# Performance work log

Measured on AMD Instinct MI355X. Metric: run time of the kernel, lower is better.

The kernel has to match this reference:

```python
import jax, jax.numpy as jnp
import numpy as np

HEADS = 8
DIM_HEAD = 64
SCALE = DIM_HEAD ** -0.5  # q scaling
EPS = 1e-5  # channel LayerNorm eps (float32)


def setup_inputs() -> dict:
    key = jax.random.key(0)
    ks = jax.random.split(key, 4)
    B, C, H, W = 8, 256, 64, 64
    hd = HEADS * DIM_HEAD  # 512
    x = jax.random.normal(ks[0], (B, C, H, W), dtype=jnp.float32)
    w_qkv = jax.random.normal(ks[1], (3 * hd, C), dtype=jnp.float32) * 0.02  # 1x1 conv, no bias
    w_out = jax.random.normal(ks[2], (C, hd), dtype=jnp.float32) * 0.02     # 1x1 conv
    b_out = jax.random.normal(ks[3], (C,), dtype=jnp.float32) * 0.02
    g_ln = jnp.ones((C,), dtype=jnp.float32)  # LayerNorm gamma
    return {"x": x, "w_qkv": w_qkv, "w_out": w_out, "b_out": b_out, "g_ln": g_ln}


def reference(x, w_qkv, w_out, b_out, g_ln):
    B, C, H, W = x.shape
    n = H * W
    hd = HEADS * DIM_HEAD
    # 1x1 conv == per-pixel matmul: [B,C,H,W] x [3hd,C] -> [B,3hd,H,W]
    qkv = jnp.einsum('bchw,oc->bohw', x, w_qkv).reshape(B, 3, HEADS, DIM_HEAD, n)
    q, k, v = qkv[:, 0], qkv[:, 1], qkv[:, 2]  # each [B,h,d,n]
    q = jax.nn.softmax(q, axis=-2) * SCALE      # softmax over head-dim d
    k = jax.nn.softmax(k, axis=-1)              # softmax over spatial n
    v = v / n
    context = jnp.einsum('bhdn,bhen->bhde', k, v)   # [B,h,d,e]
    out = jnp.einsum('bhde,bhdn->bhen', context, q)  # [B,h,e,n]
    out = out.reshape(B, hd, H, W)
    # to_out: 1x1 conv + bias, then channel-wise LayerNorm (gamma only)
    y = jnp.einsum('bchw,oc->bohw', out, w_out) + b_out[None, :, None, None]
    mean = jnp.mean(y, axis=1, keepdims=True)
    var = jnp.var(y, axis=1, keepdims=True)  # unbiased=False
    return (y - mean) * jax.lax.rsqrt(var + EPS) * g_ln[None, :, None, None]
```

## Files before the change

kernel.cpp:

```cpp
#include <hip/hip_runtime.h>
#include <stdint.h>


#define NB    8
#define CCH   256
#define NSP   4096
#define O3    1536
#define NH    8
#define DH    64
#define CSTR  136

typedef unsigned short u16;
typedef unsigned int   u32;
typedef __bf16 bf16;
typedef bf16  bf16x8 __attribute__((ext_vector_type(8)));
typedef float f32x4  __attribute__((ext_vector_type(4)));
typedef u16   u16x8  __attribute__((ext_vector_type(8)));
typedef u16   u16x4  __attribute__((ext_vector_type(4)));

__device__ __forceinline__ float b2f(u16 h) {
  union { u32 u; float f; } x; x.u = ((u32)h) << 16; return x.f;
}
__device__ __forceinline__ u16 f2b(float f) {
  union { float f; u32 u; } x; x.f = f;
  u32 r = x.u + 0x7fffu + ((x.u >> 16) & 1u);
  return (u16)(r >> 16);
}
__device__ __forceinline__ int detect_bf(const void* g) {
  return ((const u32*)g)[0] != 0x3F800000u;
}
__device__ __forceinline__ void ldg2lds16(const u16* g, u16* l) {
  __builtin_amdgcn_global_load_lds((const __attribute__((address_space(1))) void*)g,
                                   (__attribute__((address_space(3))) void*)l,
                                   16, 0, 0);
}

#define TSTR 68
__global__ __launch_bounds__(256) void k_prep(const void* __restrict__ xv,
                                              const void* __restrict__ wv,
                                              u16* __restrict__ xT,
                                              u16* __restrict__ Wb,
                                              float* __restrict__ S,
                                              float* __restrict__ ctx,
                                              const void* __restrict__ g_lnv) {
  const int isbf = detect_bf(g_lnv);
  const int t = threadIdx.x;
  if (blockIdx.z == 8) {
    const int tid = blockIdx.y * 64 + blockIdx.x;
    if (tid < 192) {
      const int idx = tid * 256 + t;
      const int row = idx >> 5, cu = idx & 31;
      int nr;
      if (row < 512)       nr = row;
      else if (row < 1024) nr = 512 + ((row - 512) >> 6) * 128 + (row & 63);
      else                 nr = 512 + ((row - 1024) >> 6) * 128 + 64 + (row & 63);
      const int didx = nr * 32 + cu;
      if (isbf) {
        reinterpret_cast<uint4*>(Wb)[didx] = reinterpret_cast<const uint4*>(wv)[idx];
      } else {
        float4 a = reinterpret_cast<const float4*>(wv)[idx * 2];
        float4 b = reinterpret_cast<const float4*>(wv)[idx * 2 + 1];
        ushort4 o0, o1;
        o0.x = f2b(a.x); o0.y = f2b(a.y); o0.z = f2b(a.z); o0.w = f2b(a.w);
        o1.x = f2b(b.x); o1.y = f2b(b.y); o1.z = f2b(b.z); o1.w = f2b(b.w);
        reinterpret_cast<ushort4*>(Wb)[didx * 2]     = o0;
        reinterpret_cast<ushort4*>(Wb)[didx * 2 + 1] = o1;
      }
    } else if (tid < 200) {
      reinterpret_cast<float2*>(S)[(tid - 192) * 256 + t] = (float2){0.f, 0.f};
    } else {
      const int base = (tid - 200) * 256 + t;
#pragma unroll
      for (int p = 0; p < 5; ++p) {
        const int i = base + p * 14336;
        if (i < 65536)
          reinterpret_cast<float4*>(ctx)[i] = (float4){0.f, 0.f, 0.f, 0.f};
      }
    }
    return;
  }
  const int b = blockIdx.z, cb = blockIdx.y * 64, nb = blockIdx.x * 64;
  __shared__ u16 tile[64 * TSTR];
  if (isbf) {
    const u16* xb = (const u16*)xv;
#pragma unroll
    for (int rr = 0; rr < 2; ++rr) {
      const int u = t + 256 * rr;
      const int c = u >> 3, ch = u & 7;
      u16x8 v = *reinterpret_cast<const u16x8*>(
          xb + ((size_t)(b * CCH + cb + c) * NSP + nb + ch * 8));
      u16* dst = tile + c * TSTR + ch * 8;
      *reinterpret_cast<u16x4*>(dst)     = (u16x4){v[0], v[1], v[2], v[3]};
      *reinterpret_cast<u16x4*>(dst + 4) = (u16x4){v[4], v[5], v[6], v[7]};
    }
  } else {
    const float* xb = (const float*)xv;
#pragma unroll
    for (int rr = 0; rr < 4; ++rr) {
      const int u = t + 256 * rr;
      const int c = u >> 4, c4 = u & 15;
      float4 f = *reinterpret_cast<const float4*>(
          xb + ((size_t)(b * CCH + cb + c) * NSP + nb + c4 * 4));
      u16x4 o; o[0] = f2b(f.x); o[1] = f2b(f.y); o[2] = f2b(f.z); o[3] = f2b(f.w);
      *reinterpret_cast<u16x4*>(tile + c * TSTR + c4 * 4) = o;
    }
  }
  __syncthreads();
#pragma unroll
  for (int rr = 0; rr < 2; ++rr) {
    const int u = t + 256 * rr;
    const int n = u >> 3, cc = u & 7;
    u16x8 o;
#pragma unroll
    for (int e = 0; e < 8; ++e) o[e] = tile[(cc * 8 + e) * TSTR + n];
    *reinterpret_cast<u16x8*>(
        xT + ((size_t)(b * NSP + nb + n) * CCH + cb + cc * 8)) = o;
  }
}

__global__ __launch_bounds__(256) void k_kv_mfma(const u16* __restrict__ Wb,
                                                 const u16* __restrict__ xT,
                                                 float* __restrict__ S,
                                                 float* __restrict__ ctx) {
  __shared__ __align__(16) u16 pool[64 * CSTR * 2];
  u16* As = pool;
  u16* Bs = pool + 4096;
  u16* ekS = pool;
  u16* vS  = pool + 64 * CSTR;

  const int b = blockIdx.z, h = blockIdx.y, n0 = blockIdx.x * 128;
  const int m0 = 512 + h * 128;
  const int t = threadIdx.x, w = t >> 6, l = t & 63;
  const int wm = (w >> 1) * 64, wn = (w & 1) * 64;
  const int fr = l & 15, quad = l >> 4;

  f32x4 acc[4][4];
#pragma unroll
  for (int i = 0; i < 4; ++i)
#pragma unroll
    for (int j = 0; j < 4; ++j) acc[i][j] = (f32x4){0.f, 0.f, 0.f, 0.f};

  {
    const u16* A = Wb;
    const u16* B = xT + (size_t)b * NSP * CCH;
    const int s0 = w * 2, s1 = s0 + 1;
    const int ra0 = s0 * 16 + (l >> 2);
    const int ra1 = s1 * 16 + (l >> 2);
    const int kc  = (l & 3) * 8;
    const int fq  = quad * 8;
    for (int k0 = 0; k0 < 256; k0 += 32) {
      ldg2lds16(A + (size_t)(m0 + ra0) * 256 + k0 + kc, As + s0 * 512);
      ldg2lds16(A + (size_t)(m0 + ra1) * 256 + k0 + kc, As + s1 * 512);
      ldg2lds16(B + (size_t)(n0 + ra0) * 256 + k0 + kc, Bs + s0 * 512);
      ldg2lds16(B + (size_t)(n0 + ra1) * 256 + k0 + kc, Bs + s1 * 512);
      asm volatile("s_waitcnt vmcnt(0)" ::: "memory");
      __syncthreads();
      bf16x8 af[4], bg[4];
#pragma unroll
      for (int i = 0; i < 4; ++i)
        af[i] = *reinterpret_cast<const bf16x8*>(As + (wm + i * 16 + fr) * 32 + fq);
#pragma unroll
      for (int j = 0; j < 4; ++j)
        bg[j] = *reinterpret_cast<const bf16x8*>(Bs + (wn + j * 16 + fr) * 32 + fq);
#pragma unroll
      for (int i = 0; i < 4; ++i)
#pragma unroll
        for (int j = 0; j < 4; ++j)
          acc[i][j] = __builtin_amdgcn_mfma_f32_16x16x32_bf16(af[i], bg[j], acc[i][j], 0, 0, 0);
      __syncthreads();
    }
  }

  {
    u16* dstT = (w < 2) ? ekS : vS;
#pragma unroll
    for (int i = 0; i < 4; ++i)
#pragma unroll
      for (int r = 0; r < 4; ++r) {
        const int row = i * 16 + quad * 4 + r;
#pragma unroll
        for (int j = 0; j < 4; ++j) {
          float v = acc[i][j][r];
          if (w < 2) v = __expf(v);
          dstT[row * CSTR + wn + j * 16 + fr] = f2b(v);
        }
      }
  }
  __syncthreads();

  {
    const int d = t >> 2, seg = t & 3;
    float s = 0.f;
    const u16* src = ekS + d * CSTR + seg * 32;
#pragma unroll
    for (int m = 0; m < 32; ++m) s += b2f(src[m]);
    s += __shfl_xor(s, 1);
    s += __shfl_xor(s, 2);
    if ((t & 3) == 0) atomicAdd(&S[b * 512 + h * 64 + d], s);
  }

  f32x4 c2[4];
#pragma unroll
  for (int j = 0; j < 4; ++j) c2[j] = (f32x4){0.f, 0.f, 0.f, 0.f};
#pragma unroll
  for (int k0 = 0; k0 < 128; k0 += 32) {
    bf16x8 af = *reinterpret_cast<const bf16x8*>(ekS + (w * 16 + fr) * CSTR + k0 + quad * 8);
#pragma unroll
    for (int j = 0; j < 4; ++j) {
      bf16x8 bg = *reinterpret_cast<const bf16x8*>(vS + (j * 16 + fr) * CSTR + k0 + quad * 8);
      c2[j] = __builtin_amdgcn_mfma_f32_16x16x32_bf16(af, bg, c2[j], 0, 0, 0);
    }
  }
  float* cb = ctx + (size_t)(b * NH + h) * 4096;
#pragma unroll
  for (int j = 0; j < 4; ++j)
#pragma unroll
    for (int r = 0; r < 4; ++r)
      atomicAdd(&cb[(w * 16 + quad * 4 + r) * 64 + j * 16 + fr], c2[j][r]);
}

__global__ __launch_bounds__(256) void k_fold(const float* __restrict__ ctx,
                                              const void* __restrict__ w_outv,
                                              const float* __restrict__ S,
                                              u16* __restrict__ Mb,
                                              const void* __restrict__ g_lnv) {
  const int isbf = detect_bf(g_lnv);
  const int h = blockIdx.x, b = blockIdx.y, ds = blockIdx.z * 16;
  const int t = threadIdx.x;
  __shared__ float ctxS[16][64];
  __shared__ float invS[16];
  if (t < 16) invS[t] = (1.0f / 4096.0f) / S[b * 512 + h * 64 + ds + t];
  {
    const float4* c4p = reinterpret_cast<const float4*>(
        ctx + (size_t)(b * NH + h) * 4096 + (size_t)ds * 64);
    float4 v = c4p[t];
    *reinterpret_cast<float4*>(&ctxS[t >> 4][(t & 15) * 4]) = v;
  }
  float wrow[64];
  if (isbf) {
    const u16* wsrc = (const u16*)w_outv + (size_t)t * 512 + h * DH;
#pragma unroll
    for (int e4 = 0; e4 < 64; e4 += 4) {
      ushort4 u = *reinterpret_cast<const ushort4*>(wsrc + e4);
      wrow[e4 + 0] = b2f(u.x); wrow[e4 + 1] = b2f(u.y);
      wrow[e4 + 2] = b2f(u.z); wrow[e4 + 3] = b2f(u.w);
    }
  } else {
    const float* wsrc = (const float*)w_outv + (size_t)t * 512 + h * DH;
#pragma unroll
    for (int e4 = 0; e4 < 64; e4 += 4) {
      float4 f = *reinterpret_cast<const float4*>(wsrc + e4);
      wrow[e4 + 0] = f.x; wrow[e4 + 1] = f.y;
      wrow[e4 + 2] = f.z; wrow[e4 + 3] = f.w;
    }
  }
  __syncthreads();
  u16* dst = Mb + ((size_t)(b * CCH + t)) * 512 + h * DH + ds;
  for (int d = 0; d < 16; ++d) {
    float s = 0.f;
#pragma unroll
    for (int e = 0; e < 64; e += 4) {
      float4 c4 = *reinterpret_cast<const float4*>(&ctxS[d][e]);
      s += wrow[e] * c4.x + wrow[e + 1] * c4.y + wrow[e + 2] * c4.z + wrow[e + 3] * c4.w;
    }
    dst[d] = f2b(s * invS[d]);
  }
}

__global__ __launch_bounds__(512, 4) void k_qmq_ln(const u16* __restrict__ Wb,
                                                   const u16* __restrict__ xT,
                                                   const u16* __restrict__ Mb,
                                                   const void* __restrict__ b_outv,
                                                   const void* __restrict__ g_lnv,
                                                   void* __restrict__ outv) {
  __shared__ __align__(16) u16 pool[64 * 512];
  __shared__ float redS[8][4][16];
  __shared__ float redQ[8][4][16];
  __shared__ float gS[256], bS[256];

  const int isbf = detect_bf(g_lnv);
  const int b  = blockIdx.y;
  const int n0 = blockIdx.x * 64;
  const int t  = threadIdx.x, w = t >> 6, l = t & 63;
  const int fr = l & 15, quad = l >> 4;

  if (t < 256) {
    gS[t] = isbf ? b2f(((const u16*)g_lnv)[t]) : ((const float*)g_lnv)[t];
    bS[t] = isbf ? b2f(((const u16*)b_outv)[t]) : ((const float*)b_outv)[t];
  }

  {
    const u16* Bg = xT + (size_t)b * NSP * CCH;
#pragma unroll
    for (int s = 0; s < 4; ++s) {
      const int p = w * 4 + s;
      const int r = 2 * p + (l >> 5);
      const int g16 = (l & 31) ^ (r & 7);
      ldg2lds16(Bg + (size_t)(n0 + r) * 256 + g16 * 8, pool + p * 512);
    }
    asm volatile("s_waitcnt vmcnt(0)" ::: "memory");
    __syncthreads();
  }

  f32x4 qa[4][4];
#pragma unroll
  for (int i = 0; i < 4; ++i)
#pragma unroll
    for (int j = 0; j < 4; ++j) qa[i][j] = (f32x4){0.f, 0.f, 0.f, 0.f};

  {
    const u16* Aq = Wb + (size_t)(w * 64 + fr) * 256 + quad * 8;
    bf16x8 afc[4], afn[4];
#pragma unroll
    for (int i = 0; i < 4; ++i)
      afc[i] = *reinterpret_cast<const bf16x8*>(Aq + (size_t)i * 16 * 256);
#pragma unroll
    for (int k0 = 0; k0 < 256; k0 += 32) {
      if (k0 + 32 < 256) {
#pragma unroll
        for (int i = 0; i < 4; ++i)
          afn[i] = *reinterpret_cast<const bf16x8*>(Aq + (size_t)i * 16 * 256 + k0 + 32);
      }
      bf16x8 bg[4];
#pragma unroll
      for (int j = 0; j < 4; ++j) {
        const int row = j * 16 + fr;
        const int c16 = (k0 >> 3) + quad;
        bg[j] = *reinterpret_cast<const bf16x8*>(
            pool + row * 256 + ((c16 ^ (row & 7)) << 3));
      }
#pragma unroll
      for (int i = 0; i < 4; ++i)
#pragma unroll
        for (int j = 0; j < 4; ++j)
          qa[i][j] = __builtin_amdgcn_mfma_f32_16x16x32_bf16(afc[i], bg[j], qa[i][j], 0, 0, 0);
      if (k0 + 32 < 256) {
#pragma unroll
        for (int i = 0; i < 4; ++i) afc[i] = afn[i];
      }
    }
  }
  __syncthreads();

#pragma unroll
  for (int j = 0; j < 4; ++j) {
    float s = 0.f;
#pragma unroll
    for (int i = 0; i < 4; ++i)
#pragma unroll
      for (int r = 0; r < 4; ++r) { qa[i][j][r] = __expf(qa[i][j][r]); s += qa[i][j][r]; }
    s += __shfl_xor(s, 16);
    s += __shfl_xor(s, 32);
    const float inv = 0.125f / s;
    const int n   = j * 16 + fr;
    const int swz = (n & 7) << 4;
#pragma unroll
    for (int i = 0; i < 4; ++i) {
      ushort4 o;
      o.x = f2b(qa[i][j][0] * inv); o.y = f2b(qa[i][j][1] * inv);
      o.z = f2b(qa[i][j][2] * inv); o.w = f2b(qa[i][j][3] * inv);
      const int hd2 = (w * 64 + i * 16 + quad * 4) * 2;
      *reinterpret_cast<ushort4*>(
          reinterpret_cast<char*>(pool) + ((n * 1024 + hd2) ^ swz)) = o;
    }
  }
  __syncthreads();

  f32x4 acc[2][4];
#pragma unroll
  for (int i = 0; i < 2; ++i)
#pragma unroll
    for (int j = 0; j < 4; ++j) acc[i][j] = (f32x4){0.f, 0.f, 0.f, 0.f};

  {
    const u16* Am = Mb + (size_t)b * CCH * 512 + (size_t)(w * 32 + fr) * 512 + quad * 8;
    bf16x8 amc[4], amn[4];
    amc[0] = *reinterpret_cast<const bf16x8*>(Am);
    amc[1] = *reinterpret_cast<const bf16x8*>(Am + 16 * 512);
    amc[2] = *reinterpret_cast<const bf16x8*>(Am + 32);
    amc[3] = *reinterpret_cast<const bf16x8*>(Am + 16 * 512 + 32);
#pragma unroll
    for (int k0 = 0; k0 < 512; k0 += 64) {
      if (k0 + 64 < 512) {
        amn[0] = *reinterpret_cast<const bf16x8*>(Am + k0 + 64);
        amn[1] = *reinterpret_cast<const bf16x8*>(Am + 16 * 512 + k0 + 64);
        amn[2] = *reinterpret_cast<const bf16x8*>(Am + k0 + 96);
        amn[3] = *reinterpret_cast<const bf16x8*>(Am + 16 * 512 + k0 + 96);
      }
      bf16x8 bg0[4], bg1[4];
#pragma unroll
      for (int j = 0; j < 4; ++j) {
        const int n = j * 16 + fr;
        const int o0 = (n * 1024 + k0 * 2 + quad * 16) ^ ((n & 7) << 4);
        const int o1 = (n * 1024 + (k0 + 32) * 2 + quad * 16) ^ ((n & 7) << 4);
        bg0[j] = *reinterpret_cast<const bf16x8*>(reinterpret_cast<const char*>(pool) + o0);
        bg1[j] = *reinterpret_cast<const bf16x8*>(reinterpret_cast<const char*>(pool) + o1);
      }
#pragma unroll
      for (int i = 0; i < 2; ++i)
#pragma unroll
        for (int j = 0; j < 4; ++j)
          acc[i][j] = __builtin_amdgcn_mfma_f32_16x16x32_bf16(amc[i], bg0[j], acc[i][j], 0, 0, 0);
#pragma unroll
      for (int i = 0; i < 2; ++i)
#pragma unroll
        for (int j = 0; j < 4; ++j)
          acc[i][j] = __builtin_amdgcn_mfma_f32_16x16x32_bf16(amc[i + 2], bg1[j], acc[i][j], 0, 0, 0);
      if (k0 + 64 < 512) {
#pragma unroll
        for (int i = 0; i < 4; ++i) amc[i] = amn[i];
      }
    }
  }

  float ps[4] = {}, pq[4] = {};
#pragma unroll
  for (int i = 0; i < 2; ++i)
#pragma unroll
    for (int r = 0; r < 4; ++r) {
      const int c = w * 32 + i * 16 + quad * 4 + r;
      const float bi = bS[c];
#pragma unroll
      for (int j = 0; j < 4; ++j) {
        acc[i][j][r] += bi;
        ps[j] += acc[i][j][r];
        pq[j] += acc[i][j][r] * acc[i][j][r];
      }
    }
#pragma unroll
  for (int j = 0; j < 4; ++j) {
    ps[j] += __shfl_xor(ps[j], 16); ps[j] += __shfl_xor(ps[j], 32);
    pq[j] += __shfl_xor(pq[j], 16); pq[j] += __shfl_xor(pq[j], 32);
  }
  if (quad == 0) {
#pragma unroll
    for (int j = 0; j < 4; ++j) { redS[w][j][fr] = ps[j]; redQ[w][j][fr] = pq[j]; }
  }
  __syncthreads();
  float mean[4], inv[4];
#pragma unroll
  for (int j = 0; j < 4; ++j) {
    float s = 0.f, q = 0.f;
#pragma unroll
    for (int g = 0; g < 8; ++g) { s += redS[g][j][fr]; q += redQ[g][j][fr]; }
    const float mn = s * (1.0f / 256.0f);
    const float vr = q * (1.0f / 256.0f) - mn * mn;
    mean[j] = mn;
    inv[j] = rsqrtf(vr + 1e-5f);
  }

#pragma unroll
  for (int i = 0; i < 2; ++i)
#pragma unroll
    for (int r = 0; r < 4; ++r) {
      const int c = w * 32 + i * 16 + quad * 4 + r;
      const float g = gS[c];
#pragma unroll
      for (int j = 0; j < 4; ++j) {
        const int col = n0 + j * 16 + fr;
        const float o = (acc[i][j][r] - mean[j]) * inv[j] * g;
        const size_t idx = ((size_t)b * CCH + c) * NSP + col;
        if (isbf) ((u16*)outv)[idx] = f2b(o);
        else      ((float*)outv)[idx] = o;
      }
    }
}

extern "C" void kernel_launch(void* const* d_in, const int* in_sizes, int n_in,
                              void* d_out, int out_size, void* d_ws, size_t ws_size,
                              hipStream_t stream) {
  (void)in_sizes; (void)n_in; (void)out_size; (void)ws_size;
  const void* x     = d_in[0];
  const void* w_qkv = d_in[1];
  const void* w_out = d_in[2];
  const void* b_out = d_in[3];
  const void* g_ln  = d_in[4];

  char* ws = (char*)d_ws;
  u16*   Wb   = (u16*)(ws + 256);
  float* S    = (float*)(ws + 851968);
  float* ctx  = (float*)(ws + 1048576);
  u16*   xT   = (u16*)(ws + 2097152);
  u16*   Mb   = (u16*)(ws + 18874368);

  k_prep    <<<dim3(64, 4, 9),  256, 0, stream>>>(x, w_qkv, xT, Wb, S, ctx, g_ln);
  k_kv_mfma <<<dim3(32, NH, NB),256, 0, stream>>>(Wb, xT, S, ctx);
  k_fold    <<<dim3(NH, NB, 4), 256, 0, stream>>>(ctx, w_out, S, Mb, g_ln);
  k_qmq_ln  <<<dim3(64, NB),    512, 0, stream>>>(Wb, xT, Mb, b_out, g_ln, d_out);
}
```

Measured before the change: 185.6 us.

## Coarsen KV kernel over four spatial tiles with double-buffered loads and partial context

Each KV block now processes four 128-column spatial tiles, with a double-buffered LDS prefetch of the next k-slice issued while the current one feeds MFMA. The context is accumulated in registers across tiles and written as 8 partial slabs without atomics. The fold kernel sums those slabs, and the ctx zeroing in the prep kernel is dropped. This cuts atomic traffic and exposed load latency, but launches a quarter as many blocks (512), which may lower occupancy, and adds extra partial-buffer reads in the fold kernel.

```diff
diff --git a/kernel.cpp b/kernel.cpp
--- a/kernel.cpp
+++ b/kernel.cpp
@@ -41,7 +41,6 @@
                                               u16* __restrict__ xT,
                                               u16* __restrict__ Wb,
                                               float* __restrict__ S,
-                                              float* __restrict__ ctx,
                                               const void* __restrict__ g_lnv) {
   const int isbf = detect_bf(g_lnv);
   const int t = threadIdx.x;
@@ -68,14 +67,6 @@
       }
     } else if (tid < 200) {
       reinterpret_cast<float2*>(S)[(tid - 192) * 256 + t] = (float2){0.f, 0.f};
-    } else {
-      const int base = (tid - 200) * 256 + t;
-#pragma unroll
-      for (int p = 0; p < 5; ++p) {
-        const int i = base + p * 14336;
-        if (i < 65536)
-          reinterpret_cast<float4*>(ctx)[i] = (float4){0.f, 0.f, 0.f, 0.f};
-      }
     }
     return;
   }
@@ -121,40 +112,65 @@
 __global__ __launch_bounds__(256) void k_kv_mfma(const u16* __restrict__ Wb,
                                                  const u16* __restrict__ xT,
                                                  float* __restrict__ S,
-                                                 float* __restrict__ ctx) {
-  __shared__ __align__(16) u16 pool[64 * CSTR * 2];
-  u16* As = pool;
-  u16* Bs = pool + 4096;
-  u16* ekS = pool;
-  u16* vS  = pool + 64 * CSTR;
-
-  const int b = blockIdx.z, h = blockIdx.y, n0 = blockIdx.x * 128;
+                                                 float* __restrict__ ctxp) {
+  __shared__ __align__(16) u16 gbuf[16384];
+  __shared__ __align__(16) u16 epi[64 * CSTR * 2];
+  u16* ekS = epi;
+  u16* vS  = epi + 64 * CSTR;
+
+  const int b = blockIdx.z, h = blockIdx.y, g = blockIdx.x;
   const int m0 = 512 + h * 128;
   const int t = threadIdx.x, w = t >> 6, l = t & 63;
   const int wm = (w >> 1) * 64, wn = (w & 1) * 64;
   const int fr = l & 15, quad = l >> 4;
 
-  f32x4 acc[4][4];
-#pragma unroll
-  for (int i = 0; i < 4; ++i)
-#pragma unroll
-    for (int j = 0; j < 4; ++j) acc[i][j] = (f32x4){0.f, 0.f, 0.f, 0.f};
-
-  {
-    const u16* A = Wb;
-    const u16* B = xT + (size_t)b * NSP * CCH;
-    const int s0 = w * 2, s1 = s0 + 1;
-    const int ra0 = s0 * 16 + (l >> 2);
-    const int ra1 = s1 * 16 + (l >> 2);
-    const int kc  = (l & 3) * 8;
-    const int fq  = quad * 8;
-    for (int k0 = 0; k0 < 256; k0 += 32) {
-      ldg2lds16(A + (size_t)(m0 + ra0) * 256 + k0 + kc, As + s0 * 512);
-      ldg2lds16(A + (size_t)(m0 + ra1) * 256 + k0 + kc, As + s1 * 512);
-      ldg2lds16(B + (size_t)(n0 + ra0) * 256 + k0 + kc, Bs + s0 * 512);
-      ldg2lds16(B + (size_t)(n0 + ra1) * 256 + k0 + kc, Bs + s1 * 512);
-      asm volatile("s_waitcnt vmcnt(0)" ::: "memory");
-      __syncthreads();
+  const u16* A = Wb;
+  const u16* B = xT + (size_t)b * NSP * CCH;
+  const int s0 = w * 2, s1 = s0 + 1;
+  const int ra0 = s0 * 16 + (l >> 2);
+  const int ra1 = s1 * 16 + (l >> 2);
+  const int kc  = (l & 3) * 8;
+  const int fq  = quad * 8;
+
+  f32x4 c2[4];
+#pragma unroll
+  for (int j = 0; j < 4; ++j) c2[j] = (f32x4){0.f, 0.f, 0.f, 0.f};
+  float sacc = 0.f;
+
+#define STAGE_KV(SUB, KK, BUF)                                                  \
+  {                                                                             \
+    const int n0_ = g * 512 + (SUB) * 128;                                      \
+    const int k0_ = (KK) * 32;                                                  \
+    u16* As_ = gbuf + (BUF) * 8192;                                             \
+    u16* Bs_ = As_ + 4096;                                                      \
+    ldg2lds16(A + (size_t)(m0 + ra0) * 256 + k0_ + kc, As_ + s0 * 512);         \
+    ldg2lds16(A + (size_t)(m0 + ra1) * 256 + k0_ + kc, As_ + s1 * 512);         \
+    ldg2lds16(B + (size_t)(n0_ + ra0) * 256 + k0_ + kc, Bs_ + s0 * 512);        \
+    ldg2lds16(B + (size_t)(n0_ + ra1) * 256 + k0_ + kc, Bs_ + s1 * 512);        \
+  }
+
+  STAGE_KV(0, 0, 0);
+
+  for (int sub = 0; sub < 4; ++sub) {
+    f32x4 acc[4][4];
+#pragma unroll
+    for (int i = 0; i < 4; ++i)
+#pragma unroll
+      for (int j = 0; j < 4; ++j) acc[i][j] = (f32x4){0.f, 0.f, 0.f, 0.f};
+
+#pragma unroll
+    for (int kk = 0; kk < 8; ++kk) {
+      if (!(sub == 3 && kk == 7)) {
+        const int ns = (kk < 7) ? sub : sub + 1;
+        const int nk = (kk < 7) ? kk + 1 : 0;
+        STAGE_KV(ns, nk, (kk + 1) & 1);
+        asm volatile("s_waitcnt vmcnt(4)" ::: "memory");
+      } else {
+        asm volatile("s_waitcnt vmcnt(0)" ::: "memory");
+      }
+      __builtin_amdgcn_s_barrier();
+      const u16* As = gbuf + (kk & 1) * 8192;
+      const u16* Bs = As + 4096;
       bf16x8 af[4], bg[4];
 #pragma unroll
       for (int i = 0; i < 4; ++i)
@@ -167,59 +183,60 @@
 #pragma unroll
         for (int j = 0; j < 4; ++j)
           acc[i][j] = __builtin_amdgcn_mfma_f32_16x16x32_bf16(af[i], bg[j], acc[i][j], 0, 0, 0);
-      __syncthreads();
-    }
-  }
-
-  {
-    u16* dstT = (w < 2) ? ekS : vS;
-#pragma unroll
-    for (int i = 0; i < 4; ++i)
-#pragma unroll
-      for (int r = 0; r < 4; ++r) {
-        const int row = i * 16 + quad * 4 + r;
-#pragma unroll
-        for (int j = 0; j < 4; ++j) {
-          float v = acc[i][j][r];
-          if (w < 2) v = __expf(v);
-          dstT[row * CSTR + wn + j * 16 + fr] = f2b(v);
+      __builtin_amdgcn_s_barrier();
+    }
+
+    {
+      u16* dstT = (w < 2) ? ekS : vS;
+#pragma unroll
+      for (int i = 0; i < 4; ++i)
+#pragma unroll
+        for (int r = 0; r < 4; ++r) {
+          const int row = i * 16 + quad * 4 + r;
+#pragma unroll
+          for (int j = 0; j < 4; ++j) {
+            float v = acc[i][j][r];
+            if (w < 2) v = __expf(v);
+            dstT[row * CSTR + wn + j * 16 + fr] = f2b(v);
+          }
         }
-      }
-  }
-  __syncthreads();
-
-  {
-    const int d = t >> 2, seg = t & 3;
-    float s = 0.f;
-    const u16* src = ekS + d * CSTR + seg * 32;
-#pragma unroll
-    for (int m = 0; m < 32; ++m) s += b2f(src[m]);
-    s += __shfl_xor(s, 1);
-    s += __shfl_xor(s, 2);
-    if ((t & 3) == 0) atomicAdd(&S[b * 512 + h * 64 + d], s);
-  }
-
-  f32x4 c2[4];
-#pragma unroll
-  for (int j = 0; j < 4; ++j) c2[j] = (f32x4){0.f, 0.f, 0.f, 0.f};
-#pragma unroll
-  for (int k0 = 0; k0 < 128; k0 += 32) {
-    bf16x8 af = *reinterpret_cast<const bf16x8*>(ekS + (w * 16 + fr) * CSTR + k0 + quad * 8);
-#pragma unroll
-    for (int j = 0; j < 4; ++j) {
-      bf16x8 bg = *reinterpret_cast<const bf16x8*>(vS + (j * 16 + fr) * CSTR + k0 + quad * 8);
-      c2[j] = __builtin_amdgcn_mfma_f32_16x16x32_bf16(af, bg, c2[j], 0, 0, 0);
-    }
-  }
-  float* cb = ctx + (size_t)(b * NH + h) * 4096;
+    }
+    asm volatile("s_waitcnt lgkmcnt(0)" ::: "memory");
+    __builtin_amdgcn_s_barrier();
+
+    {
+      const int d = t >> 2, seg = t & 3;
+      float s = 0.f;
+      const u16* src = ekS + d * CSTR + seg * 32;
+#pragma unroll
+      for (int m = 0; m < 32; ++m) s += b2f(src[m]);
+      s += __shfl_xor(s, 1);
+      s += __shfl_xor(s, 2);
+      sacc += s;
+    }
+
+#pragma unroll
+    for (int k0 = 0; k0 < 128; k0 += 32) {
+      bf16x8 af = *reinterpret_cast<const bf16x8*>(ekS + (w * 16 + fr) * CSTR + k0 + quad * 8);
+#pragma unroll
+      for (int j = 0; j < 4; ++j) {
+        bf16x8 bg = *reinterpret_cast<const bf16x8*>(vS + (j * 16 + fr) * CSTR + k0 + quad * 8);
+        c2[j] = __builtin_amdgcn_mfma_f32_16x16x32_bf16(af, bg, c2[j], 0, 0, 0);
+      }
+    }
+  }
+
+  float* cb = ctxp + ((size_t)g * 64 + b * NH + h) * 4096;
 #pragma unroll
   for (int j = 0; j < 4; ++j)
 #pragma unroll
     for (int r = 0; r < 4; ++r)
-      atomicAdd(&cb[(w * 16 + quad * 4 + r) * 64 + j * 16 + fr], c2[j][r]);
-}
-
-__global__ __launch_bounds__(256) void k_fold(const float* __restrict__ ctx,
+      cb[(w * 16 + quad * 4 + r) * 64 + j * 16 + fr] = c2[j][r];
+  if ((t & 3) == 0) atomicAdd(&S[b * 512 + h * 64 + (t >> 2)], sacc);
+#undef STAGE_KV
+}
+
+__global__ __launch_bounds__(256) void k_fold(const float* __restrict__ ctxp,
                                               const void* __restrict__ w_outv,
                                               const float* __restrict__ S,
                                               u16* __restrict__ Mb,
@@ -230,11 +247,15 @@
   __shared__ float ctxS[16][64];
   __shared__ float invS[16];
   if (t < 16) invS[t] = (1.0f / 4096.0f) / S[b * 512 + h * 64 + ds + t];
-  {
-    const float4* c4p = reinterpret_cast<const float4*>(
-        ctx + (size_t)(b * NH + h) * 4096 + (size_t)ds * 64);
-    float4 v = c4p[t];
-    *reinterpret_cast<float4*>(&ctxS[t >> 4][(t & 15) * 4]) = v;
+  const size_t bhoff = (size_t)(b * NH + h) * 4096 + (size_t)ds * 64;
+#pragma unroll
+  for (int i = 0; i < 4; ++i) {
+    const int idx = t + 256 * i;
+    float s = 0.f;
+#pragma unroll
+    for (int ch = 0; ch < 8; ++ch)
+      s += ctxp[(size_t)ch * 64 * 4096 + bhoff + idx];
+    ctxS[idx >> 6][idx & 63] = s;
   }
   float wrow[64];
   if (isbf) {
@@ -479,12 +500,12 @@
   char* ws = (char*)d_ws;
   u16*   Wb   = (u16*)(ws + 256);
   float* S    = (float*)(ws + 851968);
-  float* ctx  = (float*)(ws + 1048576);
-  u16*   xT   = (u16*)(ws + 2097152);
-  u16*   Mb   = (u16*)(ws + 18874368);
-
-  k_prep    <<<dim3(64, 4, 9),  256, 0, stream>>>(x, w_qkv, xT, Wb, S, ctx, g_ln);
-  k_kv_mfma <<<dim3(32, NH, NB),256, 0, stream>>>(Wb, xT, S, ctx);
-  k_fold    <<<dim3(NH, NB, 4), 256, 0, stream>>>(ctx, w_out, S, Mb, g_ln);
+  u16*   xT   = (u16*)(ws + 1048576);
+  float* ctxp = (float*)(ws + 17825792);
+  u16*   Mb   = (u16*)(ws + 26214400);
+
+  k_prep    <<<dim3(64, 4, 9),  256, 0, stream>>>(x, w_qkv, xT, Wb, S, g_ln);
+  k_kv_mfma <<<dim3(8, NH, NB), 256, 0, stream>>>(Wb, xT, S, ctxp);
+  k_fold    <<<dim3(NH, NB, 4), 256, 0, stream>>>(ctxp, w_out, S, Mb, g_ln);
   k_qmq_ln  <<<dim3(64, NB),    512, 0, stream>>>(Wb, xT, Mb, b_out, g_ln, d_out);
 }
```

After: 169.8 us. -8.5%, faster.
